# Kernel optimization log

Measured on AMD Instinct MI355X. Metric: run time of the kernel, lower is better.

The kernel has to match this reference:

```python
import jax, jax.numpy as jnp
import numpy as np

N = 100000      # nodes
E = 3200000     # edges (avg degree 32)
F_IN = 512      # input features
H = 16          # hidden (module default)
C = 40          # classes


def _linear_params(key, fan_in, fan_out):
    # torch.nn.Linear default init: U(-1/sqrt(fan_in), 1/sqrt(fan_in))
    k1, k2 = jax.random.split(key)
    lim = 1.0 / np.sqrt(fan_in)
    W = jax.random.uniform(k1, (fan_in, fan_out), jnp.float32, -lim, lim)
    b = jax.random.uniform(k2, (fan_out,), jnp.float32, -lim, lim)
    return W, b


def setup_inputs() -> dict:
    key = jax.random.key(0)
    ks = jax.random.split(key, 8)
    x = jax.random.normal(ks[0], (N, F_IN), jnp.float32)
    edge_index = jax.random.randint(ks[1], (2, E), 0, N, dtype=jnp.int64)
    edge_weight = jax.random.uniform(ks[2], (E,), jnp.float32)
    W_first, b_first = _linear_params(ks[3], F_IN, H)
    W_conv1, b_conv1 = _linear_params(ks[4], H, H)
    W_conv2, b_conv2 = _linear_params(ks[5], H, H)
    W_out, b_out = _linear_params(ks[6], H, C)
    return {
        "x": x, "edge_index": edge_index, "edge_weight": edge_weight,
        "W_first": W_first, "b_first": b_first,
        "W_conv1": W_conv1, "b_conv1": b_conv1,
        "W_conv2": W_conv2, "b_conv2": b_conv2,
        "W_out": W_out, "b_out": b_out,
    }


def _gcn_conv(x, W, b, row, col, ew):
    # PyG GCNConv: h = x @ W; out_i = sum_{(j->i)} norm_e * h_j + b
    # norm_e = deg^-1/2[row] * w_e * deg^-1/2[col], deg from target (col) index,
    # with self-loops (weight 1) already appended to row/col/ew.
    n = x.shape[0]
    deg = jax.ops.segment_sum(ew, col, num_segments=n)
    dinv = jnp.where(deg > 0, jax.lax.rsqrt(deg), 0.0)
    norm = dinv[row] * ew * dinv[col]
    h = x @ W
    out = jax.ops.segment_sum(h[row] * norm[:, None], col, num_segments=n)
    return out + b


def reference(x, edge_index, edge_weight, W_first, b_first,
              W_conv1, b_conv1, W_conv2, b_conv2, W_out, b_out):
    n = x.shape[0]
    # add self-loops once (shared by all conv layers)
    loop = jnp.arange(n, dtype=edge_index.dtype)
    row = jnp.concatenate([edge_index[0], loop])
    col = jnp.concatenate([edge_index[1], loop])
    ew = jnp.concatenate([edge_weight, jnp.ones((n,), edge_weight.dtype)])

    h = jax.nn.relu(x @ W_first + b_first)
    # dropout: eval mode -> identity
    h = jax.nn.relu(_gcn_conv(h, W_conv1, b_conv1, row, col, ew))
    h = jax.nn.relu(_gcn_conv(h, W_conv2, b_conv2, row, col, ew))
    # dropout: eval mode -> identity
    logits = h @ W_out + b_out
    return jax.nn.log_softmax(logits, axis=-1)
```

## Files before the change

kernel.cpp:

```cpp
#include <hip/hip_runtime.h>
#include <hip/hip_bf16.h>
#include <math.h>

#define F_IN 512
#define H 16
#define COUT 40
#define BSH 7
#define BNODES (1 << BSH)
#define SSH 12
#define EPT 64
#define CAP 5376
#define SEG 4096
#define SL 33


__global__ __launch_bounds__(256) void hist_kernel(const int* __restrict__ col,
                                                   int* __restrict__ bcnt, int E, int NBUCK) {
    extern __shared__ int hs[];
    const int t = threadIdx.x;
    for (int i = t; i < NBUCK; i += 256) hs[i] = 0;
    __syncthreads();
    long long e0 = (long long)blockIdx.x * (256 * EPT) + t;
#pragma unroll 4
    for (int k = 0; k < EPT; ++k) {
        long long e = e0 + (long long)k * 256;
        if (e < E) atomicAdd(&hs[col[e] >> BSH], 1);
    }
    __syncthreads();
    for (int i = t; i < NBUCK; i += 256) {
        int h = hs[i];
        if (h > 0) atomicAdd(&bcnt[i], h);
    }
}

__global__ void bscan_kernel(const int* __restrict__ bcnt, int* __restrict__ bbase,
                             int* __restrict__ sbase, int* __restrict__ rowptr,
                             int NBUCK, int nsup, int E, int N) {
    __shared__ int sm[1024];
    int t = threadIdx.x;
    int v = (t < NBUCK) ? bcnt[t] : 0;
    sm[t] = v;
    __syncthreads();
    for (int o = 1; o < 1024; o <<= 1) {
        int u = (t >= o) ? sm[t - o] : 0;
        __syncthreads();
        sm[t] += u;
        __syncthreads();
    }
    if (t < NBUCK) bbase[t] = sm[t] - v;
    if (t == 0) { bbase[NBUCK] = E; rowptr[N] = E; }
    __syncthreads();
    if (t < nsup) {
        int bk = t << (SSH - BSH);
        sbase[t] = (bk < NBUCK) ? (sm[bk] - bcnt[bk]) : E;
    }
    if (t == nsup) sbase[nsup] = E;
}


__global__ __launch_bounds__(256) void scat1_kernel(const int* __restrict__ row,
                                                    const int* __restrict__ col,
                                                    const float* __restrict__ ew,
                                                    const int* __restrict__ sbase,
                                                    int* __restrict__ sfill,
                                                    int2* __restrict__ ptmp, int E, int nsup) {
    __shared__ int2 stg[SEG];
    __shared__ unsigned char sup[SEG];
    __shared__ int cnt[32], base[32];
    const int t = threadIdx.x;
    const int e0 = blockIdx.x * SEG;
    int m = E - e0; if (m > SEG) m = SEG;
    if (t < 32) cnt[t] = 0;
    __syncthreads();
    for (int i = t; i < m; i += 256) {
        int e = e0 + i;
        int c = col[e];
        int s = c >> SSH;
        sup[i] = (unsigned char)s;
        atomicAdd(&cnt[s], 1);
        stg[i] = make_int2(row[e] | ((c & ((1 << SSH) - 1)) << 17), __float_as_int(ew[e]));
    }
    __syncthreads();
    if (t < nsup) {
        int h = cnt[t];
        base[t] = h ? atomicAdd(&sfill[t], h) : 0;
        cnt[t] = 0;
    }
    __syncthreads();
    for (int i = t; i < m; i += 256) {
        int s = sup[i];
        int rk = atomicAdd(&cnt[s], 1);
        ptmp[sbase[s] + base[s] + rk] = stg[i];
    }
}


__global__ __launch_bounds__(256) void scat2_kernel(const int* __restrict__ sbase,
                                                    const int* __restrict__ bbase,
                                                    int* __restrict__ ffill,
                                                    const int2* __restrict__ ptmp,
                                                    int2* __restrict__ packed, int NBUCK) {
    __shared__ int2 stg[SEG];
    __shared__ int cnt[32], base[32];
    const int t = threadIdx.x;
    const int s  = blockIdx.x / SL;
    const int sl = blockIdx.x % SL;
    const int ss = sbase[s];
    const int len = sbase[s + 1] - ss;
    const int lo = ss + (int)((long long)len * sl / SL);
    const int hi = ss + (int)((long long)len * (sl + 1) / SL);
    int m = hi - lo; if (m > SEG) m = SEG;
    if (t < 32) cnt[t] = 0;
    __syncthreads();
    for (int i = t; i < m; i += 256) {
        int2 p = ptmp[lo + i];
        stg[i] = p;
        int bk5 = ((unsigned)p.x >> (17 + BSH)) & 31;
        atomicAdd(&cnt[bk5], 1);
    }
    __syncthreads();
    if (t < 32) {
        int bk = (s << 5) + t;
        int h = cnt[t];
        base[t] = (h && bk < NBUCK) ? atomicAdd(&ffill[bk], h) : 0;
        cnt[t] = 0;
    }
    __syncthreads();
    for (int i = t; i < m; i += 256) {
        int2 p = stg[i];
        int bk5 = ((unsigned)p.x >> (17 + BSH)) & 31;
        int rk = atomicAdd(&cnt[bk5], 1);
        int bk = (s << 5) + bk5;
        packed[bbase[bk] + base[bk5] + rk] = make_int2(p.x & 0xFFFFFF, p.y);
    }
}

__global__ __launch_bounds__(256) void pass2_kernel(const int* __restrict__ bbase,
                                                    int2* __restrict__ packed,
                                                    int* __restrict__ rowptr,
                                                    float* __restrict__ dinv, int N) {
    __shared__ int2  edg[CAP];
    __shared__ int   ncnt[BNODES], nsc[BNODES], nfill[BNODES];
    __shared__ float dsum[BNODES];
    const int t = threadIdx.x;
    const int b = blockIdx.x;
    const int s = bbase[b];
    int cnt = bbase[b + 1] - s;
    if (cnt > CAP) cnt = CAP;

    for (int i = t; i < cnt; i += 256) edg[i] = packed[s + i];
    if (t < BNODES) { ncnt[t] = 0; nfill[t] = 0; dsum[t] = 0.f; }
    __syncthreads();

    for (int i = t; i < cnt; i += 256) {
        int lc = (edg[i].x >> 17) & (BNODES - 1);
        atomicAdd(&ncnt[lc], 1);
        atomicAdd(&dsum[lc], __int_as_float(edg[i].y));
    }
    __syncthreads();
    if (t < BNODES) nsc[t] = ncnt[t];
    __syncthreads();
    for (int o = 1; o < BNODES; o <<= 1) {
        int v = (t < BNODES && t >= o) ? nsc[t - o] : 0;
        __syncthreads();
        if (t < BNODES) nsc[t] += v;
        __syncthreads();
    }
    if (t < BNODES) {
        int n = b * BNODES + t;
        if (n < N) {
            rowptr[n] = s + nsc[t] - ncnt[t];
            dinv[n]   = rsqrtf(1.0f + dsum[t]);
        }
    }
    __syncthreads();
    for (int i = t; i < cnt; i += 256) {
        int lc = (edg[i].x >> 17) & (BNODES - 1);
        int rk = atomicAdd(&nfill[lc], 1);
        packed[s + nsc[lc] - ncnt[lc] + rk] = make_int2(edg[i].x & 0x1FFFF, edg[i].y);
    }
}


#define L1_ROWS 8
#define XS_CH 36
#define XS_ROW (16 * XS_CH)

__global__ __launch_bounds__(256) void l1_kernel(const float* __restrict__ x,
                                                 const float* __restrict__ W,
                                                 const float* __restrict__ b,
                                                 const float* __restrict__ dinv,
                                                 float* __restrict__ g0, int N) {
    __shared__ float xs[L1_ROWS][XS_ROW];
    __shared__ float part[L1_ROWS][256];
    const int t  = threadIdx.x;
    const int o  = t & 15;
    const int fg = t >> 4;

    float Wreg[32];
#pragma unroll
    for (int j = 0; j < 32; ++j) Wreg[j] = W[(fg * 32 + j) * H + o];
    const float bias = b[o];

    const int nbatch = (N + L1_ROWS - 1) / L1_ROWS;
    for (int batch = blockIdx.x; batch < nbatch; batch += gridDim.x) {
        const int row0 = batch * L1_ROWS;
#pragma unroll
        for (int bq = 0; bq < 4; ++bq) {
            int L  = bq * 256 + t;
            int rl = L >> 7;
            int f4 = L & 127;
            int r  = row0 + rl;
            float4 v = make_float4(0.f, 0.f, 0.f, 0.f);
            if (r < N) v = *(const float4*)&x[(size_t)r * F_IN + f4 * 4];
            int fgs = f4 >> 3, j4 = f4 & 7;
            *(float4*)&xs[rl][fgs * XS_CH + j4 * 4] = v;
        }
        __syncthreads();

        float acc[L1_ROWS];
#pragma unroll
        for (int r = 0; r < L1_ROWS; ++r) acc[r] = 0.f;
#pragma unroll
        for (int j4 = 0; j4 < 8; ++j4) {
#pragma unroll
            for (int r = 0; r < L1_ROWS; ++r) {
                float4 xv = *(const float4*)&xs[r][fg * XS_CH + j4 * 4];
                acc[r] = fmaf(xv.x, Wreg[j4 * 4 + 0], acc[r]);
                acc[r] = fmaf(xv.y, Wreg[j4 * 4 + 1], acc[r]);
                acc[r] = fmaf(xv.z, Wreg[j4 * 4 + 2], acc[r]);
                acc[r] = fmaf(xv.w, Wreg[j4 * 4 + 3], acc[r]);
            }
        }
#pragma unroll
        for (int r = 0; r < L1_ROWS; ++r) part[r][fg * 16 + o] = acc[r];
        __syncthreads();

        if (t < 128) {
            int r = t >> 4, oo = t & 15;
            float s = 0.f;
#pragma unroll
            for (int g = 0; g < 16; ++g) s += part[r][g * 16 + oo];
            s = fmaxf(s + bias, 0.f);
            int rr = row0 + r;
            if (rr < N) g0[(size_t)rr * H + oo] = s * dinv[rr];
        }
        __syncthreads();
    }
}


template<bool LAST>
__global__ __launch_bounds__(256) void conv_kernel(const int* __restrict__ rowptr,
                                                   const int2* __restrict__ packed,
                                                   const float* __restrict__ g_in,
                                                   const float* __restrict__ dinv,
                                                   const float* __restrict__ Wc,
                                                   const float* __restrict__ bc,
                                                   const float* __restrict__ Wo,
                                                   const float* __restrict__ bo,
                                                   float* __restrict__ out, int N) {
    __shared__ float Wcs[H * H];
    __shared__ float bcs[H];
    __shared__ float Wos[H * 48];
    __shared__ float bos[48];
    const int tt = threadIdx.x;
    if (tt < H * H) Wcs[tt] = Wc[tt];
    if (tt < H) bcs[tt] = bc[tt];
    if (LAST) {
        for (int i = tt; i < H * 48; i += 256) {
            int f = i / 48, c = i % 48;
            Wos[i] = (c < COUT) ? Wo[f * COUT + c] : 0.f;
        }
        if (tt < 48) bos[tt] = (tt < COUT) ? bo[tt] : 0.f;
    }
    __syncthreads();

    int t = blockIdx.x * 256 + tt;
    int n = t >> 4, o = t & 15;
    if (n >= N) return;

    int s = rowptr[n], e = rowptr[n + 1];
    float acc = g_in[(size_t)n * H + o];
    int i = s;
    for (; i + 4 <= e; i += 4) {
        int2 p0 = packed[i],     p1 = packed[i + 1];
        int2 p2 = packed[i + 2], p3 = packed[i + 3];
        float h0 = g_in[(size_t)p0.x * H + o];
        float h1 = g_in[(size_t)p1.x * H + o];
        float h2 = g_in[(size_t)p2.x * H + o];
        float h3 = g_in[(size_t)p3.x * H + o];
        acc = fmaf(__int_as_float(p0.y), h0, acc);
        acc = fmaf(__int_as_float(p1.y), h1, acc);
        acc = fmaf(__int_as_float(p2.y), h2, acc);
        acc = fmaf(__int_as_float(p3.y), h3, acc);
    }
    for (; i < e; ++i) {
        int2 p = packed[i];
        acc = fmaf(__int_as_float(p.y), g_in[(size_t)p.x * H + o], acc);
    }
    const float di = dinv[n];
    const float y = di * acc;

    float h = bcs[o];
#pragma unroll
    for (int f = 0; f < H; ++f) {
        float yf = __shfl(y, f, 16);
        h = fmaf(yf, Wcs[f * H + o], h);
    }
    h = fmaxf(h, 0.f);

    if (!LAST) {
        out[(size_t)n * H + o] = di * h;
    } else {
        float l0 = bos[o], l1 = bos[o + 16], l2 = bos[o + 32];
#pragma unroll
        for (int f = 0; f < H; ++f) {
            float hf = __shfl(h, f, 16);
            l0 = fmaf(hf, Wos[f * 48 + o], l0);
            l1 = fmaf(hf, Wos[f * 48 + o + 16], l1);
            l2 = fmaf(hf, Wos[f * 48 + o + 32], l2);
        }
        float m = fmaxf(l0, l1);
        if (o < 8) m = fmaxf(m, l2);
#pragma unroll
        for (int d = 1; d < 16; d <<= 1) m = fmaxf(m, __shfl_xor(m, d, 16));
        float sx = __expf(l0 - m) + __expf(l1 - m) + ((o < 8) ? __expf(l2 - m) : 0.f);
#pragma unroll
        for (int d = 1; d < 16; d <<= 1) sx += __shfl_xor(sx, d, 16);
        float lse = m + __logf(sx);
        out[(size_t)n * COUT + o]      = l0 - lse;
        out[(size_t)n * COUT + o + 16] = l1 - lse;
        if (o < 8) out[(size_t)n * COUT + o + 32] = l2 - lse;
    }
}


extern "C" void kernel_launch(void* const* d_in, const int* in_sizes, int n_in,
                              void* d_out, int out_size, void* d_ws, size_t ws_size,
                              hipStream_t stream) {
    const float* x       = (const float*)d_in[0];
    const int*   ei      = (const int*)d_in[1];
    const float* ew      = (const float*)d_in[2];
    const float* W_first = (const float*)d_in[3];
    const float* b_first = (const float*)d_in[4];
    const float* W_c1    = (const float*)d_in[5];
    const float* b_c1    = (const float*)d_in[6];
    const float* W_c2    = (const float*)d_in[7];
    const float* b_c2    = (const float*)d_in[8];
    const float* W_o     = (const float*)d_in[9];
    const float* b_o     = (const float*)d_in[10];

    const int N = in_sizes[0] / F_IN;
    const int E = in_sizes[2];
    const int NBUCK = (N + BNODES - 1) >> BSH;
    const int NSUP  = ((N - 1) >> SSH) + 1;
    const int HB    = (E + 256 * EPT - 1) / (256 * EPT);
    const int SB    = (E + SEG - 1) / SEG;

    const int* row = ei;
    const int* col = ei + E;

    char* wsb = (char*)d_ws;
    int*   bcnt   = (int*)wsb;                  wsb += (size_t)NBUCK * 4;
    int*   sfill  = (int*)wsb;                  wsb += (size_t)32 * 4;
    int*   ffill  = (int*)wsb;                  wsb += (size_t)NBUCK * 4;
    int*   bbase  = (int*)wsb;                  wsb += (size_t)(NBUCK + 1) * 4;
    int*   sbase  = (int*)wsb;                  wsb += (size_t)(NSUP + 1) * 4;
    int*   rowptr = (int*)wsb;                  wsb += (size_t)(N + 1) * 4;
    float* dinv   = (float*)wsb;                wsb += (size_t)N * 4;
    int2*  packed = (int2*)wsb;                 wsb += (size_t)E * 8;
    int2*  ptmp   = (int2*)wsb;                 wsb += (size_t)E * 8;
    float* g0     = (float*)ptmp;
    float* g1     = (float*)ptmp + (size_t)N * H;

    hipMemsetAsync(bcnt, 0, (size_t)(NBUCK * 2 + 32) * 4, stream);

    hist_kernel<<<HB, 256, NBUCK * 4, stream>>>(col, bcnt, E, NBUCK);
    bscan_kernel<<<1, 1024, 0, stream>>>(bcnt, bbase, sbase, rowptr, NBUCK, NSUP, E, N);
    scat1_kernel<<<SB, 256, 0, stream>>>(row, col, ew, sbase, sfill, ptmp, E, NSUP);
    scat2_kernel<<<NSUP * SL, 256, 0, stream>>>(sbase, bbase, ffill, ptmp, packed, NBUCK);
    pass2_kernel<<<NBUCK, 256, 0, stream>>>(bbase, packed, rowptr, dinv, N);

    l1_kernel<<<1024, 256, 0, stream>>>(x, W_first, b_first, dinv, g0, N);

    conv_kernel<false><<<(N * 16 + 255) / 256, 256, 0, stream>>>(
        rowptr, packed, g0, dinv, W_c1, b_c1, nullptr, nullptr, g1, N);

    conv_kernel<true><<<(N * 16 + 255) / 256, 256, 0, stream>>>(
        rowptr, packed, g1, dinv, W_c2, b_c2, W_o, b_o, (float*)d_out, N);
}
```

Measured before the change: 575.6 us.

## Replace two-level bucket sort CSR build with direct per-node atomic counting sort

Replaces the multi-pass bucketed CSR construction (histogram, superbucket scatter, bucket scatter, in-block per-node sort) with a per-node global-atomic histogram, a three-kernel exclusive scan, and a single direct atomic scatter into CSR slots. Degree normalization moves to a separate per-node kernel that sums edge weights by walking each node's CSR range. This drops the intermediate ptmp pass and the LDS staging, at the cost of scattered global atomics and uncoalesced 8-byte writes across the whole packed array. Edge order within a row is now nondeterministic, so float summation order can vary between runs.

Measured after the change: 837.9 us. +45.6%, slower.

```diff
diff --git a/kernel.cpp b/kernel.cpp
--- a/kernel.cpp
+++ b/kernel.cpp
@@ -5,40 +5,27 @@
 #define F_IN 512
 #define H 16
 #define COUT 40
-#define BSH 7
-#define BNODES (1 << BSH)
-#define SSH 12
-#define EPT 64
-#define CAP 5376
-#define SEG 4096
-#define SL 33
-
-
-__global__ __launch_bounds__(256) void hist_kernel(const int* __restrict__ col,
-                                                   int* __restrict__ bcnt, int E, int NBUCK) {
-    extern __shared__ int hs[];
-    const int t = threadIdx.x;
-    for (int i = t; i < NBUCK; i += 256) hs[i] = 0;
-    __syncthreads();
-    long long e0 = (long long)blockIdx.x * (256 * EPT) + t;
-#pragma unroll 4
-    for (int k = 0; k < EPT; ++k) {
-        long long e = e0 + (long long)k * 256;
-        if (e < E) atomicAdd(&hs[col[e] >> BSH], 1);
-    }
-    __syncthreads();
-    for (int i = t; i < NBUCK; i += 256) {
-        int h = hs[i];
-        if (h > 0) atomicAdd(&bcnt[i], h);
-    }
-}
-
-__global__ void bscan_kernel(const int* __restrict__ bcnt, int* __restrict__ bbase,
-                             int* __restrict__ sbase, int* __restrict__ rowptr,
-                             int NBUCK, int nsup, int E, int N) {
+
+
+__global__ __launch_bounds__(256) void hist2_kernel(const int* __restrict__ col,
+                                                    int* __restrict__ ncnt, int E) {
+    int i = (blockIdx.x * 256 + threadIdx.x) * 4;
+    if (i + 4 <= E) {
+        int4 c = *(const int4*)&col[i];
+        atomicAdd(&ncnt[c.x], 1);
+        atomicAdd(&ncnt[c.y], 1);
+        atomicAdd(&ncnt[c.z], 1);
+        atomicAdd(&ncnt[c.w], 1);
+    } else {
+        for (; i < E; ++i) atomicAdd(&ncnt[col[i]], 1);
+    }
+}
+
+__global__ void scanA_kernel(const int* __restrict__ ncnt, int* __restrict__ rowptr,
+                             int* __restrict__ bsum, int N) {
     __shared__ int sm[1024];
-    int t = threadIdx.x;
-    int v = (t < NBUCK) ? bcnt[t] : 0;
+    int t = threadIdx.x, n = blockIdx.x * 1024 + t;
+    int v = (n < N) ? ncnt[n] : 0;
     sm[t] = v;
     __syncthreads();
     for (int o = 1; o < 1024; o <<= 1) {
@@ -47,138 +34,71 @@
         sm[t] += u;
         __syncthreads();
     }
-    if (t < NBUCK) bbase[t] = sm[t] - v;
-    if (t == 0) { bbase[NBUCK] = E; rowptr[N] = E; }
+    if (n < N) rowptr[n] = sm[t] - v;
+    if (t == 1023) bsum[blockIdx.x] = sm[t];
+}
+
+__global__ void scanB_kernel(int* __restrict__ bsum, int nsb) {
+    __shared__ int sm[128];
+    int t = threadIdx.x;
+    int v = (t < nsb) ? bsum[t] : 0;
+    sm[t] = v;
     __syncthreads();
-    if (t < nsup) {
-        int bk = t << (SSH - BSH);
-        sbase[t] = (bk < NBUCK) ? (sm[bk] - bcnt[bk]) : E;
-    }
-    if (t == nsup) sbase[nsup] = E;
-}
-
-
-__global__ __launch_bounds__(256) void scat1_kernel(const int* __restrict__ row,
-                                                    const int* __restrict__ col,
-                                                    const float* __restrict__ ew,
-                                                    const int* __restrict__ sbase,
-                                                    int* __restrict__ sfill,
-                                                    int2* __restrict__ ptmp, int E, int nsup) {
-    __shared__ int2 stg[SEG];
-    __shared__ unsigned char sup[SEG];
-    __shared__ int cnt[32], base[32];
-    const int t = threadIdx.x;
-    const int e0 = blockIdx.x * SEG;
-    int m = E - e0; if (m > SEG) m = SEG;
-    if (t < 32) cnt[t] = 0;
-    __syncthreads();
-    for (int i = t; i < m; i += 256) {
-        int e = e0 + i;
-        int c = col[e];
-        int s = c >> SSH;
-        sup[i] = (unsigned char)s;
-        atomicAdd(&cnt[s], 1);
-        stg[i] = make_int2(row[e] | ((c & ((1 << SSH) - 1)) << 17), __float_as_int(ew[e]));
-    }
-    __syncthreads();
-    if (t < nsup) {
-        int h = cnt[t];
-        base[t] = h ? atomicAdd(&sfill[t], h) : 0;
-        cnt[t] = 0;
-    }
-    __syncthreads();
-    for (int i = t; i < m; i += 256) {
-        int s = sup[i];
-        int rk = atomicAdd(&cnt[s], 1);
-        ptmp[sbase[s] + base[s] + rk] = stg[i];
-    }
-}
-
-
-__global__ __launch_bounds__(256) void scat2_kernel(const int* __restrict__ sbase,
-                                                    const int* __restrict__ bbase,
-                                                    int* __restrict__ ffill,
-                                                    const int2* __restrict__ ptmp,
-                                                    int2* __restrict__ packed, int NBUCK) {
-    __shared__ int2 stg[SEG];
-    __shared__ int cnt[32], base[32];
-    const int t = threadIdx.x;
-    const int s  = blockIdx.x / SL;
-    const int sl = blockIdx.x % SL;
-    const int ss = sbase[s];
-    const int len = sbase[s + 1] - ss;
-    const int lo = ss + (int)((long long)len * sl / SL);
-    const int hi = ss + (int)((long long)len * (sl + 1) / SL);
-    int m = hi - lo; if (m > SEG) m = SEG;
-    if (t < 32) cnt[t] = 0;
-    __syncthreads();
-    for (int i = t; i < m; i += 256) {
-        int2 p = ptmp[lo + i];
-        stg[i] = p;
-        int bk5 = ((unsigned)p.x >> (17 + BSH)) & 31;
-        atomicAdd(&cnt[bk5], 1);
-    }
-    __syncthreads();
-    if (t < 32) {
-        int bk = (s << 5) + t;
-        int h = cnt[t];
-        base[t] = (h && bk < NBUCK) ? atomicAdd(&ffill[bk], h) : 0;
-        cnt[t] = 0;
-    }
-    __syncthreads();
-    for (int i = t; i < m; i += 256) {
-        int2 p = stg[i];
-        int bk5 = ((unsigned)p.x >> (17 + BSH)) & 31;
-        int rk = atomicAdd(&cnt[bk5], 1);
-        int bk = (s << 5) + bk5;
-        packed[bbase[bk] + base[bk5] + rk] = make_int2(p.x & 0xFFFFFF, p.y);
-    }
-}
-
-__global__ __launch_bounds__(256) void pass2_kernel(const int* __restrict__ bbase,
-                                                    int2* __restrict__ packed,
-                                                    int* __restrict__ rowptr,
-                                                    float* __restrict__ dinv, int N) {
-    __shared__ int2  edg[CAP];
-    __shared__ int   ncnt[BNODES], nsc[BNODES], nfill[BNODES];
-    __shared__ float dsum[BNODES];
-    const int t = threadIdx.x;
-    const int b = blockIdx.x;
-    const int s = bbase[b];
-    int cnt = bbase[b + 1] - s;
-    if (cnt > CAP) cnt = CAP;
-
-    for (int i = t; i < cnt; i += 256) edg[i] = packed[s + i];
-    if (t < BNODES) { ncnt[t] = 0; nfill[t] = 0; dsum[t] = 0.f; }
-    __syncthreads();
-
-    for (int i = t; i < cnt; i += 256) {
-        int lc = (edg[i].x >> 17) & (BNODES - 1);
-        atomicAdd(&ncnt[lc], 1);
-        atomicAdd(&dsum[lc], __int_as_float(edg[i].y));
-    }
-    __syncthreads();
-    if (t < BNODES) nsc[t] = ncnt[t];
-    __syncthreads();
-    for (int o = 1; o < BNODES; o <<= 1) {
-        int v = (t < BNODES && t >= o) ? nsc[t - o] : 0;
-        __syncthreads();
-        if (t < BNODES) nsc[t] += v;
-        __syncthreads();
-    }
-    if (t < BNODES) {
-        int n = b * BNODES + t;
-        if (n < N) {
-            rowptr[n] = s + nsc[t] - ncnt[t];
-            dinv[n]   = rsqrtf(1.0f + dsum[t]);
-        }
-    }
-    __syncthreads();
-    for (int i = t; i < cnt; i += 256) {
-        int lc = (edg[i].x >> 17) & (BNODES - 1);
-        int rk = atomicAdd(&nfill[lc], 1);
-        packed[s + nsc[lc] - ncnt[lc] + rk] = make_int2(edg[i].x & 0x1FFFF, edg[i].y);
-    }
+    for (int o = 1; o < 128; o <<= 1) {
+        int u = (t >= o) ? sm[t - o] : 0;
+        __syncthreads();
+        sm[t] += u;
+        __syncthreads();
+    }
+    if (t < nsb) bsum[t] = sm[t] - v;
+}
+
+__global__ __launch_bounds__(256) void scanC_kernel(int* __restrict__ rowptr,
+                                                    const int* __restrict__ bsum,
+                                                    int N, int E) {
+    int n = blockIdx.x * 256 + threadIdx.x;
+    if (n < N) rowptr[n] += bsum[n >> 10];
+    if (n == N) rowptr[N] = E;
+}
+
+__global__ __launch_bounds__(256) void scatter_kernel(const int* __restrict__ row,
+                                                      const int* __restrict__ col,
+                                                      const float* __restrict__ ew,
+                                                      const int* __restrict__ rowptr,
+                                                      int* __restrict__ fill,
+                                                      int2* __restrict__ packed, int E) {
+    int i = (blockIdx.x * 256 + threadIdx.x) * 4;
+    if (i + 4 <= E) {
+        int4 c = *(const int4*)&col[i];
+        int4 r = *(const int4*)&row[i];
+        float4 w = *(const float4*)&ew[i];
+        int b0 = rowptr[c.x], b1 = rowptr[c.y], b2 = rowptr[c.z], b3 = rowptr[c.w];
+        int k0 = atomicAdd(&fill[c.x], 1);
+        int k1 = atomicAdd(&fill[c.y], 1);
+        int k2 = atomicAdd(&fill[c.z], 1);
+        int k3 = atomicAdd(&fill[c.w], 1);
+        packed[b0 + k0] = make_int2(r.x, __float_as_int(w.x));
+        packed[b1 + k1] = make_int2(r.y, __float_as_int(w.y));
+        packed[b2 + k2] = make_int2(r.z, __float_as_int(w.z));
+        packed[b3 + k3] = make_int2(r.w, __float_as_int(w.w));
+    } else {
+        for (; i < E; ++i) {
+            int c = col[i];
+            int k = atomicAdd(&fill[c], 1);
+            packed[rowptr[c] + k] = make_int2(row[i], __float_as_int(ew[i]));
+        }
+    }
+}
+
+__global__ __launch_bounds__(256) void dinv_kernel(const int* __restrict__ rowptr,
+                                                   const int2* __restrict__ packed,
+                                                   float* __restrict__ dinv, int N) {
+    int n = blockIdx.x * 256 + threadIdx.x;
+    if (n >= N) return;
+    int s = rowptr[n], e = rowptr[n + 1];
+    float sum = 1.0f;
+    for (int i = s; i < e; ++i) sum += __int_as_float(packed[i].y);
+    dinv[n] = rsqrtf(sum);
 }
 
 
@@ -353,34 +273,31 @@
 
     const int N = in_sizes[0] / F_IN;
     const int E = in_sizes[2];
-    const int NBUCK = (N + BNODES - 1) >> BSH;
-    const int NSUP  = ((N - 1) >> SSH) + 1;
-    const int HB    = (E + 256 * EPT - 1) / (256 * EPT);
-    const int SB    = (E + SEG - 1) / SEG;
 
     const int* row = ei;
     const int* col = ei + E;
 
+    const int NB1024 = (N + 1023) / 1024;
+    const int GB4    = (E / 4 + 255) / 256;
+
     char* wsb = (char*)d_ws;
-    int*   bcnt   = (int*)wsb;                  wsb += (size_t)NBUCK * 4;
-    int*   sfill  = (int*)wsb;                  wsb += (size_t)32 * 4;
-    int*   ffill  = (int*)wsb;                  wsb += (size_t)NBUCK * 4;
-    int*   bbase  = (int*)wsb;                  wsb += (size_t)(NBUCK + 1) * 4;
-    int*   sbase  = (int*)wsb;                  wsb += (size_t)(NSUP + 1) * 4;
+    int*   ncnt   = (int*)wsb;                  wsb += (size_t)N * 4;
+    int*   fill   = (int*)wsb;                  wsb += (size_t)N * 4;
     int*   rowptr = (int*)wsb;                  wsb += (size_t)(N + 1) * 4;
+    int*   bsum   = (int*)wsb;                  wsb += (size_t)128 * 4;
     float* dinv   = (float*)wsb;                wsb += (size_t)N * 4;
     int2*  packed = (int2*)wsb;                 wsb += (size_t)E * 8;
-    int2*  ptmp   = (int2*)wsb;                 wsb += (size_t)E * 8;
-    float* g0     = (float*)ptmp;
-    float* g1     = (float*)ptmp + (size_t)N * H;
-
-    hipMemsetAsync(bcnt, 0, (size_t)(NBUCK * 2 + 32) * 4, stream);
-
-    hist_kernel<<<HB, 256, NBUCK * 4, stream>>>(col, bcnt, E, NBUCK);
-    bscan_kernel<<<1, 1024, 0, stream>>>(bcnt, bbase, sbase, rowptr, NBUCK, NSUP, E, N);
-    scat1_kernel<<<SB, 256, 0, stream>>>(row, col, ew, sbase, sfill, ptmp, E, NSUP);
-    scat2_kernel<<<NSUP * SL, 256, 0, stream>>>(sbase, bbase, ffill, ptmp, packed, NBUCK);
-    pass2_kernel<<<NBUCK, 256, 0, stream>>>(bbase, packed, rowptr, dinv, N);
+    float* g0     = (float*)wsb;                wsb += (size_t)N * H * 4;
+    float* g1     = (float*)wsb;                wsb += (size_t)N * H * 4;
+
+    hipMemsetAsync(ncnt, 0, (size_t)2 * N * 4, stream);
+
+    hist2_kernel<<<GB4, 256, 0, stream>>>(col, ncnt, E);
+    scanA_kernel<<<NB1024, 1024, 0, stream>>>(ncnt, rowptr, bsum, N);
+    scanB_kernel<<<1, 128, 0, stream>>>(bsum, NB1024);
+    scanC_kernel<<<(N + 256) / 256, 256, 0, stream>>>(rowptr, bsum, N, E);
+    scatter_kernel<<<GB4, 256, 0, stream>>>(row, col, ew, rowptr, fill, packed, E);
+    dinv_kernel<<<(N + 255) / 256, 256, 0, stream>>>(rowptr, packed, dinv, N);
 
     l1_kernel<<<1024, 256, 0, stream>>>(x, W_first, b_first, dinv, g0, N);
 
```
